# Kernel optimization log

Hardware: AMD Instinct MI355X
Metric: run time of the kernel (lower is better)

## Reference

```python
import jax, jax.numpy as jnp
import numpy as np
import math
from jax import lax

B, C, BINS, W = 2, 8, 1024, 512
HEADS = 8
HD = BINS // HEADS            # 128 head dim
ROT = HD // 2                 # rotary rot_dim = bins//num_heads//2 = 64


def setup_inputs() -> dict:
    key = jax.random.key(0)
    k1, k2, k3, k4, k5 = jax.random.split(key, 5)
    s_lin = 1.0 / math.sqrt(BINS)
    return {
        "x": jax.random.normal(k1, (B, C, BINS, W), dtype=jnp.float32),
        "Wq_lin": jax.random.uniform(k2, (C, BINS, BINS), jnp.float32, -s_lin, s_lin),
        "Wq_conv": jax.random.normal(k3, (C, C, 1, 3), dtype=jnp.float32) * 0.1,
        "bq_conv": jax.random.normal(k4, (C,), dtype=jnp.float32) * 0.1,
        "Wout": jax.random.uniform(k5, (C, BINS, BINS), jnp.float32, -s_lin, s_lin),
    }


def _mc_linear(x, Wc):
    # separable MultichannelLinear: out[b,c,o,w] = sum_i W[c,o,i] x[b,c,i,w]
    return jnp.einsum('coi,bciw->bcow', Wc, x)


def _proj(x, Wl, Wc, bc):
    y = _mc_linear(x, Wl)
    y = lax.conv_general_dilated(y, Wc, (1, 1), ((0, 0), (1, 1)),
                                 dimension_numbers=('NCHW', 'OIHW', 'NCHW'))
    return y + bc[None, :, None, None]


def _to_heads(y):
    # [b,c,bins,w] -> [b,c,H,w,hd]
    b, c, _, w = y.shape
    return y.transpose(0, 1, 3, 2).reshape(b, c, w, HEADS, HD).transpose(0, 1, 3, 2, 4)


def _rotary(t):
    # lucidrains RotaryEmbedding(dim=ROT, freqs_for='lang'): rotate first ROT dims over seq axis (-2)
    inv = 1.0 / (10000.0 ** (jnp.arange(0, ROT, 2, dtype=jnp.float32) / ROT))  # [ROT//2]
    pos = jnp.arange(t.shape[-2], dtype=jnp.float32)
    f = jnp.repeat(pos[:, None] * inv[None, :], 2, axis=-1)  # [w, ROT] interleaved repeat
    cos, sin = jnp.cos(f), jnp.sin(f)
    left, right = t[..., :ROT], t[..., ROT:]
    x1, x2 = left[..., 0::2], left[..., 1::2]
    rot = jnp.stack([-x2, x1], axis=-1).reshape(left.shape)
    return jnp.concatenate([left * cos + rot * sin, right], axis=-1)


def reference(x, Wq_lin, Wq_conv, bq_conv, Wout):
    b, c, h, w = x.shape
    # NOTE: original forward uses q_proj for q, k AND v (k_proj/v_proj unused)
    qp = _proj(x, Wq_lin, Wq_conv, bq_conv)
    qh = _to_heads(qp)                       # [b,c,H,w,hd]
    q = _rotary(qh)
    k = _rotary(qh)
    v = qh
    scale = 1.0 / math.sqrt(h)               # custom scale: sqrt(bins), not sqrt(head_dim)
    qk = jnp.einsum('bchqd,bchkd->bchqk', q, k) * scale
    a = jnp.einsum('bchqk,bchkd->bchqd', jax.nn.softmax(qk, axis=-1), v)
    # [b,c,H,w,hd] -> [b,c,bins,w]
    a = a.transpose(0, 1, 3, 2, 4).reshape(b, c, w, h).transpose(0, 1, 3, 2)
    return _mc_linear(a, Wout)
```

## Files before the change

kernel.cpp:

```cpp
#include <hip/hip_runtime.h>
#include <cstddef>

#define Bb 2
#define Cc_ 8
#define BINS 1024
#define Ww 512
#define HEADS 8
#define HD 128
#define NELEM (Bb*Cc_*BINS*Ww)
#define SLOT ((size_t)NELEM + 640)

typedef __attribute__((ext_vector_type(8)))  __bf16 bf16x8;
typedef __attribute__((ext_vector_type(4)))  __bf16 bf16x4;
typedef __attribute__((ext_vector_type(4)))  float  f32x4;
typedef __attribute__((ext_vector_type(16))) float  f32x16;
#define MFMA32(a,b,c) __builtin_amdgcn_mfma_f32_32x32x16_bf16(a,b,c,0,0,0)

__device__ __forceinline__ void async16(const __bf16* g, __bf16* l) {
    __builtin_amdgcn_global_load_lds(
        (const __attribute__((address_space(1))) void*)g,
        (__attribute__((address_space(3))) void*)l, 16, 0, 0);
}

__global__ void __launch_bounds__(256) xpose(const float* __restrict__ x,
                                             __bf16* __restrict__ xT) {
    int b2 = blockIdx.x;
    int t = threadIdx.x;
    int w0 = (b2 & 7) * 64;
    int i0 = ((b2 >> 3) & 15) * 64;
    int bc = b2 >> 7;
    const float* src = x + (size_t)bc * BINS * Ww;
    __bf16* dst = xT + (size_t)bc * Ww * BINS;
    __shared__ float T[64][65];
    #pragma unroll
    for (int pass = 0; pass < 4; pass++) {
        int idx = t + pass * 256;
        int il = idx >> 4, ch = idx & 15;
        f32x4 v = __builtin_nontemporal_load(
            (const f32x4*)&src[(size_t)(i0 + il) * Ww + w0 + ch * 4]);
        T[il][ch * 4 + 0] = v[0]; T[il][ch * 4 + 1] = v[1];
        T[il][ch * 4 + 2] = v[2]; T[il][ch * 4 + 3] = v[3];
    }
    __syncthreads();
    #pragma unroll
    for (int pass = 0; pass < 2; pass++) {
        int idx = t + pass * 256;
        int wl = idx >> 3, ch = idx & 7;
        bf16x8 o;
        #pragma unroll
        for (int j = 0; j < 8; j++) o[j] = (__bf16)T[ch * 8 + j][wl];
        *(bf16x8*)&dst[(size_t)(w0 + wl) * BINS + i0 + ch * 8] = o;
    }
}

template<bool BF16OUT>
__global__ void __launch_bounds__(256) gemm32(const float* __restrict__ Wall,
                                              const __bf16* __restrict__ Bt,
                                              void* __restrict__ Yv) {
    int bc = blockIdx.z, c = bc & 7;
    const float*  A  = Wall + (size_t)c  * BINS * BINS;
    const __bf16* Bm = Bt   + (size_t)bc * Ww * BINS;
    int n0 = blockIdx.x * 128, m0 = blockIdx.y * 128;

    __shared__ __align__(16) char smem[32768];
    __bf16* Asm = (__bf16*)smem;
    __bf16* Bsm = (__bf16*)(smem + 16384);

    int t = threadIdx.x, w = t >> 6, l = t & 63;
    int l31 = l & 31, h = l >> 5;
    int wm = w >> 1, wn = w & 1;

    int rowS[4], colS[4];
    #pragma unroll
    for (int j = 0; j < 4; j++) {
        int p = j * 256 + t;
        int r = p >> 3, cs = (p & 7) ^ (r & 7);
        rowS[j] = r; colS[j] = cs * 8;
    }

    f32x16 acc[2][2];
    #pragma unroll
    for (int a = 0; a < 2; a++)
        #pragma unroll
        for (int b = 0; b < 2; b++)
            #pragma unroll
            for (int r = 0; r < 16; r++) acc[a][b][r] = 0.f;

    for (int k0 = 0; k0 < BINS; k0 += 64) {
        __syncthreads();
        #pragma unroll
        for (int j = 0; j < 4; j++) {
            async16(Bm + (size_t)(n0 + rowS[j]) * BINS + k0 + colS[j],
                    Bsm + (j * 256 + t) * 8);
            const float* ap = A + (size_t)(m0 + rowS[j]) * BINS + k0 + colS[j];
            f32x4 lo = *(const f32x4*)ap;
            f32x4 hi = *(const f32x4*)(ap + 4);
            bf16x8 o = {(__bf16)lo[0], (__bf16)lo[1], (__bf16)lo[2], (__bf16)lo[3],
                        (__bf16)hi[0], (__bf16)hi[1], (__bf16)hi[2], (__bf16)hi[3]};
            *(bf16x8*)&Asm[(j * 256 + t) * 8] = o;
        }
        __syncthreads();
        bf16x8 af[2][4], bfr[2][4];
        #pragma unroll
        for (int mt = 0; mt < 2; mt++)
            #pragma unroll
            for (int kc = 0; kc < 4; kc++) {
                int row = wm * 64 + mt * 32 + l31;
                int ch = (kc * 2 + h) ^ (row & 7);
                af[mt][kc] = *(bf16x8*)&Asm[row * 64 + ch * 8];
            }
        #pragma unroll
        for (int nt = 0; nt < 2; nt++)
            #pragma unroll
            for (int kc = 0; kc < 4; kc++) {
                int row = wn * 64 + nt * 32 + l31;
                int ch = (kc * 2 + h) ^ (row & 7);
                bfr[nt][kc] = *(bf16x8*)&Bsm[row * 64 + ch * 8];
            }
        #pragma unroll
        for (int kc = 0; kc < 4; kc++)
            #pragma unroll
            for (int mt = 0; mt < 2; mt++)
                #pragma unroll
                for (int nt = 0; nt < 2; nt++)
                    acc[mt][nt] = MFMA32(af[mt][kc], bfr[nt][kc], acc[mt][nt]);
    }

    __syncthreads();
    if constexpr (BF16OUT) {
        __bf16* Ob = (__bf16*)smem;
        __bf16* Cm = (__bf16*)Yv + (size_t)bc * BINS * Ww;
        #pragma unroll
        for (int mt = 0; mt < 2; mt++)
            #pragma unroll
            for (int nt = 0; nt < 2; nt++)
                #pragma unroll
                for (int reg = 0; reg < 16; reg++) {
                    int ml = wm * 64 + mt * 32 + (reg & 3) + 8 * (reg >> 2) + 4 * h;
                    int nl = wn * 64 + nt * 32 + l31;
                    Ob[ml * 128 + nl] = (__bf16)acc[mt][nt][reg];
                }
        __syncthreads();
        #pragma unroll
        for (int pass = 0; pass < 8; pass++) {
            int idx = t + pass * 256;
            int row = idx >> 4, ch = idx & 15;
            *(bf16x8*)&Cm[(size_t)(m0 + row) * Ww + n0 + ch * 8] =
                *(bf16x8*)&Ob[row * 128 + ch * 8];
        }
    } else {
        float* Of = (float*)smem;
        float* Cm = (float*)Yv + (size_t)bc * BINS * Ww;
        #pragma unroll
        for (int half = 0; half < 2; half++) {
            if (wm == half) {
                #pragma unroll
                for (int mt = 0; mt < 2; mt++)
                    #pragma unroll
                    for (int nt = 0; nt < 2; nt++)
                        #pragma unroll
                        for (int reg = 0; reg < 16; reg++) {
                            int ml = mt * 32 + (reg & 3) + 8 * (reg >> 2) + 4 * h;
                            int nl = wn * 64 + nt * 32 + l31;
                            Of[ml * 128 + nl] = acc[mt][nt][reg];
                        }
            }
            __syncthreads();
            #pragma unroll
            for (int pass = 0; pass < 8; pass++) {
                int idx = t + pass * 256;
                int row = idx >> 5, c4 = idx & 31;
                __builtin_nontemporal_store(
                    *(const f32x4*)&Of[row * 128 + c4 * 4],
                    (f32x4*)&Cm[(size_t)(m0 + half * 64 + row) * Ww + n0 + c4 * 4]);
            }
            __syncthreads();
        }
    }
}

__global__ void __launch_bounds__(256) conv1x3_reg(const __bf16* __restrict__ y,
                                                   const float* __restrict__ Wc,
                                                   const float* __restrict__ bias,
                                                   __bf16* __restrict__ vt) {
    int tid = blockIdx.x * 256 + threadIdx.x;
    int wc = tid & 63;
    int h  = (tid >> 6) & 1023;
    int b  = tid >> 16;
    int w0 = wc * 8;

    float ym[8][8], yl[8], yr[8];
    #pragma unroll
    for (int ci = 0; ci < 8; ci++) {
        const __bf16* row = y + ((size_t)(b * 8 + ci) * BINS + h) * Ww;
        bf16x8 v = *(const bf16x8*)&row[w0];
        #pragma unroll
        for (int j = 0; j < 8; j++) ym[ci][j] = (float)v[j];
        yl[ci] = (w0 > 0)   ? (float)row[w0 - 1] : 0.f;
        yr[ci] = (w0 < 504) ? (float)row[w0 + 8] : 0.f;
    }
    #pragma unroll
    for (int co = 0; co < 8; co++) {
        float acc[8];
        float bv = bias[co];
        #pragma unroll
        for (int j = 0; j < 8; j++) acc[j] = bv;
        #pragma unroll
        for (int ci = 0; ci < 8; ci++) {
            float wa = Wc[(co * 8 + ci) * 3 + 0];
            float wb = Wc[(co * 8 + ci) * 3 + 1];
            float wcc = Wc[(co * 8 + ci) * 3 + 2];
            acc[0] += yl[ci] * wa;
            #pragma unroll
            for (int j = 1; j < 8; j++) acc[j] += ym[ci][j - 1] * wa;
            #pragma unroll
            for (int j = 0; j < 8; j++) acc[j] += ym[ci][j] * wb;
            #pragma unroll
            for (int j = 0; j < 7; j++) acc[j] += ym[ci][j + 1] * wcc;
            acc[7] += yr[ci] * wcc;
        }
        bf16x8 o;
        #pragma unroll
        for (int j = 0; j < 8; j++) o[j] = (__bf16)acc[j];
        *(bf16x8*)&vt[((size_t)(b * 8 + co) * BINS + h) * Ww + w0] = o;
    }
}

__global__ void __launch_bounds__(256) rotary_transpose(const __bf16* __restrict__ vt,
                                                        __bf16* __restrict__ qrot) {
    int p0  = blockIdx.x * 64;
    int bch = blockIdx.y;
    int t = threadIdx.x;
    __shared__ float T[64 * 129];

    const __bf16* src = vt + (size_t)bch * HD * Ww;
    for (int pass = 0; pass < 4; pass++) {
        int idx = t + pass * 256;
        int d = idx >> 3, ch = idx & 7;
        bf16x8 v = *(const bf16x8*)&src[(size_t)d * Ww + p0 + ch * 8];
        #pragma unroll
        for (int j = 0; j < 8; j++) T[(ch * 8 + j) * 129 + d] = (float)v[j];
    }
    __syncthreads();
    for (int pass = 0; pass < 4; pass++) {
        int idx = t + pass * 256;
        int p = idx >> 4, chunk = idx & 15;
        float pos = (float)(p0 + p);
        bf16x8 o;
        if (chunk < 8) {
            #pragma unroll
            for (int j = 0; j < 8; j += 2) {
                int d = chunk * 8 + j;
                int jj = d >> 1;
                float inv = __expf(-(2.0f * jj / 64.0f) * 9.210340371976184f);
                float sn, cs;
                __sincosf(pos * inv, &sn, &cs);
                float x1 = T[p * 129 + d];
                float x2 = T[p * 129 + d + 1];
                o[j]     = (__bf16)(x1 * cs - x2 * sn);
                o[j + 1] = (__bf16)(x2 * cs + x1 * sn);
            }
        } else {
            #pragma unroll
            for (int j = 0; j < 8; j++)
                o[j] = (__bf16)T[p * 129 + chunk * 8 + j];
        }
        *(bf16x8*)&qrot[((size_t)bch * Ww + p0 + p) * HD + chunk * 8] = o;
    }
}

__global__ void __launch_bounds__(256, 2) attn32(const __bf16* __restrict__ qrot,
                                                 const __bf16* __restrict__ vt,
                                                 __bf16* __restrict__ attnT) {
    int bid = blockIdx.x;
    int bch = bid & 127, q0 = (bid >> 7) * 128;
    int t = threadIdx.x, wv = t >> 6, lane = t & 63;
    int l31 = lane & 31, h = lane >> 5;

    __shared__ __align__(16) char smem[49152];
    __bf16* Ks  = (__bf16*)smem;
    __bf16* Vts = (__bf16*)(smem + 16384);
    __bf16* Psw = (__bf16*)(smem + 32768) + wv * 2048;

    const __bf16* qb = qrot + (size_t)bch * Ww * HD;
    const __bf16* vb = vt   + (size_t)bch * HD * Ww;

    int qrow = q0 + wv * 32 + l31;
    bf16x8 qf[8];
    #pragma unroll
    for (int c = 0; c < 8; c++) {
        bf16x8 v = *(const bf16x8*)&qb[(size_t)qrow * HD + c * 16 + h * 8];
        #pragma unroll
        for (int j = 0; j < 8; j++) v[j] = (__bf16)((float)v[j] * 0.03125f);
        qf[c] = v;
    }

    f32x16 oacc[4];
    #pragma unroll
    for (int dt = 0; dt < 4; dt++)
        #pragma unroll
        for (int r = 0; r < 16; r++) oacc[dt][r] = 0.f;
    float m_st = -1e30f, l_st = 0.f;

    for (int kt = 0; kt < 8; kt++) {
        int k0 = kt * 64;
        __syncthreads();
        #pragma unroll
        for (int i = 0; i < 4; i++) {
            int p = wv * 256 + i * 64 + lane;
            int r  = p >> 4, cs  = ((p & 15) ^ (r & 15)) * 8;
            async16(qb + (size_t)(k0 + r) * HD + cs, Ks + (wv * 256 + i * 64) * 8);
            int r2 = p >> 3, cs2 = ((p & 7) ^ (r2 & 7)) * 8;
            async16(vb + (size_t)r2 * Ww + k0 + cs2, Vts + (wv * 256 + i * 64) * 8);
        }
        __syncthreads();

        f32x16 st[2];
        #pragma unroll
        for (int t2 = 0; t2 < 2; t2++)
            #pragma unroll
            for (int r = 0; r < 16; r++) st[t2][r] = 0.f;
        #pragma unroll
        for (int c = 0; c < 8; c++)
            #pragma unroll
            for (int t2 = 0; t2 < 2; t2++) {
                int row = t2 * 32 + l31;
                int ch = (c * 2 + h) ^ (row & 15);
                bf16x8 ak = *(bf16x8*)&Ks[row * 128 + ch * 8];
                st[t2] = MFMA32(ak, qf[c], st[t2]);
            }

        float mx = -1e30f;
        #pragma unroll
        for (int t2 = 0; t2 < 2; t2++)
            #pragma unroll
            for (int r = 0; r < 16; r++) mx = fmaxf(mx, st[t2][r]);
        mx = fmaxf(mx, __shfl_xor(mx, 32));
        float mnew = fmaxf(m_st, mx);
        float alpha = __expf(m_st - mnew);
        float sum = 0.f;
        #pragma unroll
        for (int t2 = 0; t2 < 2; t2++)
            #pragma unroll
            for (int r = 0; r < 16; r++) {
                float p = __expf(st[t2][r] - mnew);
                st[t2][r] = p;
                sum += p;
            }
        sum += __shfl_xor(sum, 32);
        l_st = l_st * alpha + sum;
        m_st = mnew;

        #pragma unroll
        for (int t2 = 0; t2 < 2; t2++)
            #pragma unroll
            for (int g = 0; g < 4; g++) {
                bf16x4 pk = {(__bf16)st[t2][4 * g],     (__bf16)st[t2][4 * g + 1],
                             (__bf16)st[t2][4 * g + 2], (__bf16)st[t2][4 * g + 3]};
                int ch = (t2 * 4 + g) ^ (l31 & 7);
                *(bf16x4*)&Psw[l31 * 64 + ch * 8 + 4 * h] = pk;
            }
        #pragma unroll
        for (int dt = 0; dt < 4; dt++)
            #pragma unroll
            for (int r = 0; r < 16; r++) oacc[dt][r] *= alpha;

        #pragma unroll
        for (int kc = 0; kc < 4; kc++) {
            int chp = (kc * 2 + h) ^ (l31 & 7);
            bf16x8 bp = *(bf16x8*)&Psw[l31 * 64 + chp * 8];
            #pragma unroll
            for (int dt = 0; dt < 4; dt++) {
                int row = dt * 32 + l31;
                int cv = (kc * 2 + h) ^ (row & 7);
                bf16x8 av = *(bf16x8*)&Vts[row * 64 + cv * 8];
                oacc[dt] = MFMA32(av, bp, oacc[dt]);
            }
        }
    }

    __syncthreads();
    __bf16* Ob = (__bf16*)smem + wv * 4096;
    float linv = 1.f / l_st;
    #pragma unroll
    for (int dt = 0; dt < 4; dt++)
        #pragma unroll
        for (int g = 0; g < 4; g++) {
            bf16x4 pk = {(__bf16)(oacc[dt][4 * g] * linv),
                         (__bf16)(oacc[dt][4 * g + 1] * linv),
                         (__bf16)(oacc[dt][4 * g + 2] * linv),
                         (__bf16)(oacc[dt][4 * g + 3] * linv)};
            int ch = (dt * 4 + g) ^ (l31 & 15);
            *(bf16x4*)&Ob[l31 * 128 + ch * 8 + 4 * h] = pk;
        }
    int bc = bch >> 3, h0 = bch & 7;
    #pragma unroll
    for (int i = 0; i < 8; i++) {
        int p = i * 64 + lane;
        int rr = p >> 4, cc = p & 15;
        int cs = cc ^ (rr & 15);
        bf16x8 v = *(bf16x8*)&Ob[rr * 128 + cs * 8];
        *(bf16x8*)&attnT[((size_t)bc * Ww + q0 + wv * 32 + rr) * BINS + h0 * HD + cc * 8] = v;
    }
}

extern "C" void kernel_launch(void* const* d_in, const int* in_sizes, int n_in,
                              void* d_out, int out_size, void* d_ws, size_t ws_size,
                              hipStream_t stream) {
    const float* x       = (const float*)d_in[0];
    const float* Wq_lin  = (const float*)d_in[1];
    const float* Wq_conv = (const float*)d_in[2];
    const float* bq_conv = (const float*)d_in[3];
    const float* Wout    = (const float*)d_in[4];
    float* out = (float*)d_out;

    __bf16* U = (__bf16*)d_ws;
    __bf16* xT      = U + 0 * SLOT;
    __bf16* y       = U + 1 * SLOT;
    __bf16* vtb     = U + 2 * SLOT;
    __bf16* qrot    = U + 3 * SLOT;
    __bf16* attnT   = U + 1 * SLOT;

    xpose<<<dim3(2048), 256, 0, stream>>>(x, xT);
    gemm32<true><<<dim3(Ww / 128, BINS / 128, Bb * Cc_), 256, 0, stream>>>(Wq_lin, xT, y);
    conv1x3_reg<<<dim3(Bb * BINS * 64 / 256), 256, 0, stream>>>(y, Wq_conv, bq_conv, vtb);
    rotary_transpose<<<dim3(Ww / 64, Bb * Cc_ * HEADS), 256, 0, stream>>>(vtb, qrot);
    attn32<<<dim3((Ww / 128) * 128), 256, 0, stream>>>(qrot, vtb, attnT);
    gemm32<false><<<dim3(Ww / 128, BINS / 128, Bb * Cc_), 256, 0, stream>>>(Wout, attnT, out);
}
```

Before: 243.5 us.

## Double-buffer LDS tiles in GEMM and attention kernels to overlap loads with MFMA

Both the projection GEMM and the flash-attention kernel now keep two LDS buffers per operand. The next K-tile is prefetched (async global->LDS for B/K/V, register-staged fp32 A converted after the MFMAs) while the current tile is computed, and the two barriers per iteration become one explicit waitcnt+barrier. The aim is to hide global memory latency behind matrix math. The cost is doubled LDS use (64KB GEMM, 80KB attention), which may cut occupancy, especially for attn32's launch bound of two blocks per CU. It also adds registers for the staged A values.

New measurement: 242.3 us. About the same (-0.5%).

```diff
diff --git a/kernel.cpp b/kernel.cpp
--- a/kernel.cpp
+++ b/kernel.cpp
@@ -20,6 +20,12 @@
     __builtin_amdgcn_global_load_lds(
         (const __attribute__((address_space(1))) void*)g,
         (__attribute__((address_space(3))) void*)l, 16, 0, 0);
+}
+
+__device__ __forceinline__ void phase_barrier() {
+    asm volatile("s_waitcnt vmcnt(0) lgkmcnt(0)" ::: "memory");
+    __builtin_amdgcn_s_barrier();
+    __builtin_amdgcn_sched_barrier(0);
 }
 
 __global__ void __launch_bounds__(256) xpose(const float* __restrict__ x,
@@ -62,12 +68,12 @@
     const __bf16* Bm = Bt   + (size_t)bc * Ww * BINS;
     int n0 = blockIdx.x * 128, m0 = blockIdx.y * 128;
 
-    __shared__ __align__(16) char smem[32768];
-    __bf16* Asm = (__bf16*)smem;
-    __bf16* Bsm = (__bf16*)(smem + 16384);
-
-    int t = threadIdx.x, w = t >> 6, l = t & 63;
-    int l31 = l & 31, h = l >> 5;
+    __shared__ __align__(16) char smem[65536];
+    __bf16* AsmB = (__bf16*)smem;
+    __bf16* BsmB = (__bf16*)(smem + 32768);
+
+    int t = threadIdx.x, w = t >> 6;
+    int l31 = t & 31, h = (t >> 5) & 1;
     int wm = w >> 1, wn = w & 1;
 
     int rowS[4], colS[4];
@@ -86,20 +92,46 @@
             #pragma unroll
             for (int r = 0; r < 16; r++) acc[a][b][r] = 0.f;
 
-    for (int k0 = 0; k0 < BINS; k0 += 64) {
-        __syncthreads();
-        #pragma unroll
-        for (int j = 0; j < 4; j++) {
-            async16(Bm + (size_t)(n0 + rowS[j]) * BINS + k0 + colS[j],
-                    Bsm + (j * 256 + t) * 8);
-            const float* ap = A + (size_t)(m0 + rowS[j]) * BINS + k0 + colS[j];
-            f32x4 lo = *(const f32x4*)ap;
-            f32x4 hi = *(const f32x4*)(ap + 4);
-            bf16x8 o = {(__bf16)lo[0], (__bf16)lo[1], (__bf16)lo[2], (__bf16)lo[3],
-                        (__bf16)hi[0], (__bf16)hi[1], (__bf16)hi[2], (__bf16)hi[3]};
-            *(bf16x8*)&Asm[(j * 256 + t) * 8] = o;
-        }
-        __syncthreads();
+    f32x4 alo[4], ahi[4];
+
+    #pragma unroll
+    for (int j = 0; j < 4; j++) {
+        const float* ap = A + (size_t)(m0 + rowS[j]) * BINS + colS[j];
+        alo[j] = *(const f32x4*)ap;
+        ahi[j] = *(const f32x4*)(ap + 4);
+    }
+    #pragma unroll
+    for (int j = 0; j < 4; j++)
+        async16(Bm + (size_t)(n0 + rowS[j]) * BINS + colS[j],
+                BsmB + (j * 256 + t) * 8);
+    #pragma unroll
+    for (int j = 0; j < 4; j++) {
+        bf16x8 o = {(__bf16)alo[j][0], (__bf16)alo[j][1], (__bf16)alo[j][2], (__bf16)alo[j][3],
+                    (__bf16)ahi[j][0], (__bf16)ahi[j][1], (__bf16)ahi[j][2], (__bf16)ahi[j][3]};
+        *(bf16x8*)&AsmB[(j * 256 + t) * 8] = o;
+    }
+    phase_barrier();
+
+    for (int ks = 0; ks < 16; ks++) {
+        int cur = ks & 1, nxt = cur ^ 1;
+        __bf16* Asm = AsmB + cur * 8192;
+        __bf16* Bsm = BsmB + cur * 8192;
+        bool hn = (ks + 1 < 16);
+        int k1 = (ks + 1) * 64;
+
+        if (hn) {
+            #pragma unroll
+            for (int j = 0; j < 4; j++) {
+                const float* ap = A + (size_t)(m0 + rowS[j]) * BINS + k1 + colS[j];
+                alo[j] = *(const f32x4*)ap;
+                ahi[j] = *(const f32x4*)(ap + 4);
+            }
+            #pragma unroll
+            for (int j = 0; j < 4; j++)
+                async16(Bm + (size_t)(n0 + rowS[j]) * BINS + k1 + colS[j],
+                        BsmB + nxt * 8192 + (j * 256 + t) * 8);
+        }
+
         bf16x8 af[2][4], bfr[2][4];
         #pragma unroll
         for (int mt = 0; mt < 2; mt++)
@@ -124,9 +156,18 @@
                 #pragma unroll
                 for (int nt = 0; nt < 2; nt++)
                     acc[mt][nt] = MFMA32(af[mt][kc], bfr[nt][kc], acc[mt][nt]);
-    }
-
-    __syncthreads();
+
+        if (hn) {
+            #pragma unroll
+            for (int j = 0; j < 4; j++) {
+                bf16x8 o = {(__bf16)alo[j][0], (__bf16)alo[j][1], (__bf16)alo[j][2], (__bf16)alo[j][3],
+                            (__bf16)ahi[j][0], (__bf16)ahi[j][1], (__bf16)ahi[j][2], (__bf16)ahi[j][3]};
+                *(bf16x8*)&AsmB[nxt * 8192 + (j * 256 + t) * 8] = o;
+            }
+        }
+        phase_barrier();
+    }
+
     if constexpr (BF16OUT) {
         __bf16* Ob = (__bf16*)smem;
         __bf16* Cm = (__bf16*)Yv + (size_t)bc * BINS * Ww;
@@ -277,10 +318,10 @@
     int t = threadIdx.x, wv = t >> 6, lane = t & 63;
     int l31 = lane & 31, h = lane >> 5;
 
-    __shared__ __align__(16) char smem[49152];
-    __bf16* Ks  = (__bf16*)smem;
-    __bf16* Vts = (__bf16*)(smem + 16384);
-    __bf16* Psw = (__bf16*)(smem + 32768) + wv * 2048;
+    __shared__ __align__(16) char smem[81920];
+    __bf16* KsB  = (__bf16*)smem;
+    __bf16* VtsB = (__bf16*)(smem + 32768);
+    __bf16* Psw  = (__bf16*)(smem + 65536) + wv * 2048;
 
     const __bf16* qb = qrot + (size_t)bch * Ww * HD;
     const __bf16* vb = vt   + (size_t)bch * HD * Ww;
@@ -302,18 +343,34 @@
         for (int r = 0; r < 16; r++) oacc[dt][r] = 0.f;
     float m_st = -1e30f, l_st = 0.f;
 
+    #pragma unroll
+    for (int i = 0; i < 4; i++) {
+        int p = wv * 256 + i * 64 + lane;
+        int r  = p >> 4, cs  = ((p & 15) ^ (r & 15)) * 8;
+        async16(qb + (size_t)r * HD + cs, KsB + (wv * 256 + i * 64) * 8);
+        int r2 = p >> 3, cs2 = ((p & 7) ^ (r2 & 7)) * 8;
+        async16(vb + (size_t)r2 * Ww + cs2, VtsB + (wv * 256 + i * 64) * 8);
+    }
+    phase_barrier();
+
     for (int kt = 0; kt < 8; kt++) {
-        int k0 = kt * 64;
-        __syncthreads();
-        #pragma unroll
-        for (int i = 0; i < 4; i++) {
-            int p = wv * 256 + i * 64 + lane;
-            int r  = p >> 4, cs  = ((p & 15) ^ (r & 15)) * 8;
-            async16(qb + (size_t)(k0 + r) * HD + cs, Ks + (wv * 256 + i * 64) * 8);
-            int r2 = p >> 3, cs2 = ((p & 7) ^ (r2 & 7)) * 8;
-            async16(vb + (size_t)r2 * Ww + k0 + cs2, Vts + (wv * 256 + i * 64) * 8);
-        }
-        __syncthreads();
+        int cur = kt & 1, nxt = cur ^ 1;
+        __bf16* Ks  = KsB  + cur * 8192;
+        __bf16* Vts = VtsB + cur * 8192;
+
+        if (kt < 7) {
+            int k1 = (kt + 1) * 64;
+            #pragma unroll
+            for (int i = 0; i < 4; i++) {
+                int p = wv * 256 + i * 64 + lane;
+                int r  = p >> 4, cs  = ((p & 15) ^ (r & 15)) * 8;
+                async16(qb + (size_t)(k1 + r) * HD + cs,
+                        KsB + nxt * 8192 + (wv * 256 + i * 64) * 8);
+                int r2 = p >> 3, cs2 = ((p & 7) ^ (r2 & 7)) * 8;
+                async16(vb + (size_t)r2 * Ww + k1 + cs2,
+                        VtsB + nxt * 8192 + (wv * 256 + i * 64) * 8);
+            }
+        }
 
         f32x16 st[2];
         #pragma unroll
@@ -377,9 +434,10 @@
                 oacc[dt] = MFMA32(av, bp, oacc[dt]);
             }
         }
-    }
-
-    __syncthreads();
+
+        phase_barrier();
+    }
+
     __bf16* Ob = (__bf16*)smem + wv * 4096;
     float linv = 1.f / l_st;
     #pragma unroll
```
